# Optimization experiments

Measured on AMD Instinct MI355X. Metric: run time of the kernel, lower is better.

The kernel has to match this reference:

```python
import jax, jax.numpy as jnp
import numpy as np

EPS = 1e-5
NUM_HEADS = 8

def _bn(x, w, b, m, v):
    # inference-mode BatchNorm2d over channel dim of (B,C,H,W)
    inv = w / jnp.sqrt(v + EPS)
    return x * inv[None, :, None, None] + (b - m * inv)[None, :, None, None]

def _conv1x1(x, W, b):
    # 1x1 conv == per-pixel matmul: W is (out_ch, in_ch)
    return jnp.einsum('bchw,ec->behw', x, W) + b[None, :, None, None]

def _forward(x, bn1_w, bn1_b, bn1_m, bn1_v, Wq, bq, Wk, bk, Wv, bv, gamma, temperature,
             conv_w, conv_b, cbn_w, cbn_b, cbn_m, cbn_v, rs_w, rs_b, rbn_w, rbn_b, rbn_m, rbn_v):
    B, C, Wd, Hd = x.shape
    S = Wd * Hd
    E = Wq.shape[0]
    hd = E // NUM_HEADS
    xa = jax.nn.relu(_bn(x, bn1_w, bn1_b, bn1_m, bn1_v))
    def proj(Wm, bm):
        return _conv1x1(xa, Wm, bm).reshape(B, NUM_HEADS, hd, S).transpose(0, 1, 3, 2)  # (B,h,S,d)
    q = proj(Wq, bq)
    k = proj(Wk, bk)
    v = proj(Wv, bv)
    scores = jnp.einsum('bhsd,bhtd->bhst', q, k) / temperature  # (B,h,S,S)
    scores = scores - jnp.max(scores, axis=-1, keepdims=True)   # redundant amax-subtract as in source
    attn = jax.nn.softmax(scores, axis=-1)
    out = jnp.einsum('bhst,bhtd->bhsd', attn, v)
    out = out.transpose(0, 1, 3, 2).reshape(B, E, Wd, Hd)
    conv_path = jax.nn.relu(_bn(_conv1x1(x, conv_w, conv_b), cbn_w, cbn_b, cbn_m, cbn_v))
    fused = gamma[0] * out + conv_path
    return jax.nn.gelu(_bn(_conv1x1(fused, rs_w, rs_b), rbn_w, rbn_b, rbn_m, rbn_v), approximate=False)

def setup_inputs() -> dict:
    key = jax.random.key(0)
    ks = jax.random.split(key, 18)
    C, E = 256, 512
    n = lambda k, s, sc=0.02: jax.random.normal(k, s, jnp.float32) * sc
    return {
        'x': jax.random.normal(ks[0], (1, C, 64, 64), jnp.float32),
        'bn1_w': 1.0 + n(ks[1], (C,), 0.1), 'bn1_b': n(ks[2], (C,), 0.1),
        'bn1_m': n(ks[3], (C,), 0.05), 'bn1_v': 0.5 + jax.random.uniform(ks[4], (C,), jnp.float32),
        'Wq': n(ks[5], (E, C)), 'bq': jnp.zeros((E,), jnp.float32),
        'Wk': n(ks[6], (E, C)), 'bk': jnp.zeros((E,), jnp.float32),
        'Wv': n(ks[7], (E, C)), 'bv': jnp.zeros((E,), jnp.float32),
        'gamma': jnp.full((1,), 0.5, jnp.float32),
        'temperature': jnp.asarray(0.85, jnp.float32),
        'conv_w': n(ks[8], (E, C)), 'conv_b': jnp.zeros((E,), jnp.float32),
        'cbn_w': 1.0 + n(ks[9], (E,), 0.1), 'cbn_b': n(ks[10], (E,), 0.1),
        'cbn_m': n(ks[11], (E,), 0.05), 'cbn_v': 0.5 + jax.random.uniform(ks[12], (E,), jnp.float32),
        'rs_w': n(ks[13], (C, E)), 'rs_b': jnp.zeros((C,), jnp.float32),
        'rbn_w': 1.0 + n(ks[14], (C,), 0.1), 'rbn_b': n(ks[15], (C,), 0.1),
        'rbn_m': n(ks[16], (C,), 0.05), 'rbn_v': 0.5 + jax.random.uniform(ks[17], (C,), jnp.float32),
    }

def reference(x, bn1_w, bn1_b, bn1_m, bn1_v, Wq, bq, Wk, bk, Wv, bv, gamma, temperature,
              conv_w, conv_b, cbn_w, cbn_b, cbn_m, cbn_v, rs_w, rs_b, rbn_w, rbn_b, rbn_m, rbn_v):
    return _forward(x, bn1_w, bn1_b, bn1_m, bn1_v, Wq, bq, Wk, bk, Wv, bv, gamma, temperature,
                    conv_w, conv_b, cbn_w, cbn_b, cbn_m, cbn_v, rs_w, rs_b, rbn_w, rbn_b, rbn_m, rbn_v)
```

## Files before the change

kernel.cpp:

```cpp
#include <hip/hip_runtime.h>

#define S_DIM 4096
#define C_IN  256
#define E_DIM 512
#define HD    64
#define EPSV  1e-5f

typedef __attribute__((ext_vector_type(8))) short s8v;
typedef __attribute__((ext_vector_type(4))) short s4v;
typedef __attribute__((ext_vector_type(4))) float f4v;
typedef __attribute__((ext_vector_type(16))) float f16v;

__device__ __forceinline__ float bf2f(unsigned short h){
  union{unsigned u; float f;} v; v.u = ((unsigned)h)<<16; return v.f;
}
__device__ __forceinline__ unsigned short f2bf(float f){
  union{float f; unsigned u;} v; v.f = f;
  unsigned r = v.u + 0x7fffu + ((v.u>>16)&1u);
  return (unsigned short)(r>>16);
}
__device__ __forceinline__ unsigned cvtpk_bf16(float lo, float hi_){
  unsigned r;
  asm("v_cvt_pk_bf16_f32 %0, %1, %2" : "=v"(r) : "v"(lo), "v"(hi_));
  return r;
}
__device__ __forceinline__ s8v lds_rd8(const unsigned short* b, int row, int ck){
  return *(const s8v*)&b[(row<<6) + (((ck)^(row&7))<<3)];
}
__device__ __forceinline__ void lds_wr8(unsigned short* b, int row, int ck, s8v v){
  *(s8v*)&b[(row<<6) + (((ck)^(row&7))<<3)] = v;
}
__device__ __forceinline__ s4v lds_rd4v(const unsigned short* b, int row, int q4){
  return *(const s4v*)&b[(row<<5) + (((q4) ^ ((row>>1)&7))<<2)];
}
__device__ __forceinline__ void gl_lds16(const unsigned short* g, unsigned short* l){
  __builtin_amdgcn_global_load_lds(
      (const __attribute__((address_space(1))) unsigned int*)g,
      (__attribute__((address_space(3))) unsigned int*)l, 16, 0, 0);
}

__global__ __launch_bounds__(256) void k_wcvt(const float* __restrict__ w0,
    const float* __restrict__ w1, const float* __restrict__ w2,
    const float* __restrict__ w3, const float* __restrict__ w4,
    unsigned short* __restrict__ dst){
  int i = blockIdx.x*256 + threadIdx.x;
  int z = blockIdx.y;
  const float* s = (z==0)?w0:(z==1)?w1:(z==2)?w2:(z==3)?w3:w4;
  dst[z*(E_DIM*C_IN) + i] = f2bf(s[i]);
}

__global__ __launch_bounds__(256) void k_prep(const float* __restrict__ x,
    const float* __restrict__ bw, const float* __restrict__ bb,
    const float* __restrict__ bm, const float* __restrict__ bvar,
    unsigned short* __restrict__ XaT, unsigned short* __restrict__ XrT){
  __shared__ float tile[32][33];
  int tid = threadIdx.x;
  int tx = tid & 31, ty = tid >> 5;
  int s0 = blockIdx.x*32, c0 = blockIdx.y*32;
  #pragma unroll
  for(int p=0;p<4;p++){
    int c = c0 + ty + p*8;
    tile[ty+p*8][tx] = x[c*S_DIM + s0 + tx];
  }
  __syncthreads();
  int cc = c0 + tx;
  float inv  = bw[cc] * rsqrtf(bvar[cc] + EPSV);
  float beta = bb[cc] - bm[cc]*inv;
  #pragma unroll
  for(int p=0;p<4;p++){
    int s = s0 + ty + p*8;
    float v = tile[tx][ty+p*8];
    float a = v*inv + beta; a = a>0.f?a:0.f;
    XaT[s*C_IN + cc] = f2bf(a);
    XrT[s*C_IN + cc] = f2bf(v);
  }
}

__global__ __launch_bounds__(256) void k_proj(
    const unsigned short* __restrict__ XaT, const unsigned short* __restrict__ XrT,
    const unsigned short* __restrict__ Wb,
    const float* __restrict__ bq, const float* __restrict__ bk,
    const float* __restrict__ bvb, const float* __restrict__ bc,
    const float* __restrict__ cw, const float* __restrict__ cbb,
    const float* __restrict__ cm, const float* __restrict__ cvv,
    unsigned short* __restrict__ QT, unsigned short* __restrict__ KT,
    unsigned short* __restrict__ Vx, unsigned short* __restrict__ CT){
  int z = blockIdx.z;
  const unsigned short* Xin = (z==3) ? XrT : XaT;
  const unsigned short* W   = Wb + z*(E_DIM*C_IN);
  const float* bias = (z==0)?bq:(z==1)?bk:(z==2)?bvb:bc;

  __shared__ unsigned short Als[128*64];
  __shared__ unsigned short Bls[64*64];
  int tid = threadIdx.x;
  int w = tid>>6, l = tid&63, g = l>>4, c16 = l&15;
  int wr = w>>1, wc = w&1;
  int s0 = blockIdx.x*128, e0 = blockIdx.y*64;

  f4v acc[4][2];
  #pragma unroll
  for(int m=0;m<4;m++)
    #pragma unroll
    for(int n=0;n<2;n++) acc[m][n] = (f4v){0.f,0.f,0.f,0.f};

  for(int kk=0;kk<4;kk++){
    __syncthreads();
    #pragma unroll
    for(int p=0;p<4;p++){
      int ck = p*256 + tid, row = ck>>3, ch = ck&7;
      s8v v = *(const s8v*)&Xin[(s0+row)*C_IN + kk*64 + ch*8];
      lds_wr8(Als, row, ch, v);
    }
    #pragma unroll
    for(int p=0;p<2;p++){
      int ck = p*256 + tid, row = ck>>3, ch = ck&7;
      s8v v = *(const s8v*)&W[(e0+row)*C_IN + kk*64 + ch*8];
      lds_wr8(Bls, row, ch, v);
    }
    __syncthreads();
    #pragma unroll
    for(int kb=0;kb<2;kb++){
      s8v bfr[2];
      #pragma unroll
      for(int n=0;n<2;n++) bfr[n] = lds_rd8(Bls, wc*32 + n*16 + c16, g + kb*4);
      #pragma unroll
      for(int m=0;m<4;m++){
        s8v af = lds_rd8(Als, wr*64 + m*16 + c16, g + kb*4);
        #pragma unroll
        for(int n=0;n<2;n++)
          acc[m][n] = __builtin_amdgcn_mfma_f32_16x16x32_bf16(af, bfr[n], acc[m][n], 0,0,0);
      }
    }
  }
  #pragma unroll
  for(int n=0;n<2;n++){
    int e = e0 + wc*32 + n*16 + c16;
    float bsv = bias[e];
    float cinv = 0.f, cbeta = 0.f;
    if(z==3){ cinv = cw[e]*rsqrtf(cvv[e]+EPSV); cbeta = cbb[e] - cm[e]*cinv; }
    #pragma unroll
    for(int m=0;m<4;m++){
      int sb = s0 + wr*64 + m*16 + g*4;
      if(z==2){
        s4v pk;
        #pragma unroll
        for(int i=0;i<4;i++) pk[i] = (short)f2bf(acc[m][n][i] + bsv);
        int sb2 = (sb & ~31) | ((((sb>>2)&7) ^ ((e>>1)&7))<<2);
        *(s4v*)&Vx[e*S_DIM + sb2] = pk;
      } else {
        unsigned short* dst = (z==0)?QT:(z==1)?KT:CT;
        #pragma unroll
        for(int i=0;i<4;i++){
          float vv = acc[m][n][i] + bsv;
          if(z==3){ vv = vv*cinv + cbeta; vv = vv>0.f?vv:0.f; }
          int key = sb+i;
          int ee = e;
          if(z==1) ee = (e & ~56) | ((((e>>3)&7) ^ (key&7))<<3);
          dst[key*E_DIM + ee] = f2bf(vv);
        }
      }
    }
  }
}

__global__ __launch_bounds__(256,2) void k_attn(
    const unsigned short* __restrict__ QT, const unsigned short* __restrict__ KT,
    const unsigned short* __restrict__ Vx, const unsigned short* __restrict__ CT,
    const float* __restrict__ gamma, const float* __restrict__ temp,
    unsigned short* __restrict__ fusedT){
  __shared__ unsigned short SM[32768];
  int tid = threadIdx.x;
  int kh = tid>>6, l = tid&63, l31 = l&31, hi = l>>5;
  int bx = blockIdx.x;
  int h = bx&7;
  int q0b = (bx>>3)*64;
  float scl = 1.4426950408889634f / temp[0];

  #define STAGE(B, T) { \
    int sK = kh*1024 + (T)*32; \
    _Pragma("unroll") \
    for(int j=0;j<4;j++) \
      gl_lds16(&KT[(sK + j*8 + (l>>3))*E_DIM + h*HD + (l&7)*8], \
               SM + (B)*16384 + kh*2048 + j*512); \
    _Pragma("unroll") \
    for(int j=0;j<4;j++) \
      gl_lds16(&Vx[(h*HD + j*16 + (l>>2))*S_DIM + sK + (l&3)*8], \
               SM + (B)*16384 + 8192 + kh*2048 + j*512); \
  }

  STAGE(0, 0);

  s8v qf[2][4];
  #pragma unroll
  for(int qg=0;qg<2;qg++){
    int q = q0b + qg*32 + l31;
    #pragma unroll
    for(int ks=0;ks<4;ks++){
      s8v r = *(const s8v*)&QT[q*E_DIM + h*HD + ks*16 + hi*8];
      #pragma unroll
      for(int j=0;j<8;j++) qf[qg][ks][j] = (short)f2bf(bf2f((unsigned short)r[j])*scl);
    }
  }

  f16v oacc[2][2];
  #pragma unroll
  for(int qg=0;qg<2;qg++)
    #pragma unroll
    for(int dt=0;dt<2;dt++)
      #pragma unroll
      for(int r=0;r<16;r++) oacc[qg][dt][r]=0.f;
  float lrun[2] = {0.f, 0.f};

  int buf = 0;
  #pragma unroll 1
  for(int t=0;t<32;t++){
    if(t<31){
      STAGE(buf^1, t+1);
      asm volatile("s_waitcnt vmcnt(8)" ::: "memory");
    } else {
      asm volatile("s_waitcnt vmcnt(0)" ::: "memory");
    }
    __builtin_amdgcn_s_barrier();

    const unsigned short* Kb = SM + buf*16384 + kh*2048;
    const unsigned short* Vb = SM + buf*16384 + 8192 + kh*2048;

    s8v kf[4];
    #pragma unroll
    for(int ks=0;ks<4;ks++) kf[ks] = lds_rd8(Kb, l31, ks*2 + hi);

    union{ s8v v; unsigned u[4]; } pa[2][2];
    #pragma unroll
    for(int qg=0;qg<2;qg++){
      f16v d;
      #pragma unroll
      for(int r=0;r<16;r++) d[r]=0.f;
      __builtin_amdgcn_s_setprio(1);
      #pragma unroll
      for(int ks=0;ks<4;ks++)
        d = __builtin_amdgcn_mfma_f32_32x32x16_bf16(kf[ks], qf[qg][ks], d, 0,0,0);
      __builtin_amdgcn_s_setprio(0);
      float e_[16], ls = 0.f;
      #pragma unroll
      for(int r=0;r<16;r++){ e_[r] = __builtin_amdgcn_exp2f(d[r]); ls += e_[r]; }
      lrun[qg] += ls;
      #pragma unroll
      for(int j=0;j<4;j++){
        pa[qg][0].u[j] = cvtpk_bf16(e_[2*j],   e_[2*j+1]);
        pa[qg][1].u[j] = cvtpk_bf16(e_[8+2*j], e_[8+2*j+1]);
      }
    }

    __builtin_amdgcn_s_setprio(1);
    #pragma unroll
    for(int dt=0;dt<2;dt++){
      int vr = dt*32 + l31;
      union{ s8v v; s4v h2[2]; } vf;
      vf.h2[0] = lds_rd4v(Vb, vr, hi);
      vf.h2[1] = lds_rd4v(Vb, vr, 2 + hi);
      oacc[0][dt] = __builtin_amdgcn_mfma_f32_32x32x16_bf16(pa[0][0].v, vf.v, oacc[0][dt], 0,0,0);
      oacc[1][dt] = __builtin_amdgcn_mfma_f32_32x32x16_bf16(pa[1][0].v, vf.v, oacc[1][dt], 0,0,0);
      vf.h2[0] = lds_rd4v(Vb, vr, 4 + hi);
      vf.h2[1] = lds_rd4v(Vb, vr, 6 + hi);
      oacc[0][dt] = __builtin_amdgcn_mfma_f32_32x32x16_bf16(pa[0][1].v, vf.v, oacc[0][dt], 0,0,0);
      oacc[1][dt] = __builtin_amdgcn_mfma_f32_32x32x16_bf16(pa[1][1].v, vf.v, oacc[1][dt], 0,0,0);
    }
    __builtin_amdgcn_s_setprio(0);

    __builtin_amdgcn_sched_barrier(0);
    __builtin_amdgcn_s_barrier();
    buf ^= 1;
  }

  #pragma unroll
  for(int qg=0;qg<2;qg++) lrun[qg] += __shfl_xor(lrun[qg], 32);

  float* slab = (float*)SM;
  float* l_buf = slab + 3*64*33;
  float ga = gamma[0];
  #pragma unroll
  for(int qg=0;qg<2;qg++){
    __syncthreads();
    if(kh!=0){
      float* dst = slab + (((kh-1))*64 + l)*33;
      #pragma unroll
      for(int r=0;r<16;r++){ dst[r] = oacc[qg][0][r]; dst[16+r] = oacc[qg][1][r]; }
      dst[32] = lrun[qg];
    }
    __syncthreads();
    if(kh==0){
      float lt = lrun[qg];
      #pragma unroll
      for(int s=0;s<3;s++){
        const float* src = slab + ((s)*64 + l)*33;
        #pragma unroll
        for(int r=0;r<16;r++){ oacc[qg][0][r] += src[r]; oacc[qg][1][r] += src[16+r]; }
        lt += src[32];
      }
      if(hi==0) l_buf[l31] = lt;
      #pragma unroll
      for(int dt=0;dt<2;dt++){
        int e = h*HD + dt*32 + l31;
        #pragma unroll
        for(int g4=0;g4<4;g4++){
          float4 lv = *(float4*)&l_buf[g4*8 + hi*4];
          float la[4] = {lv.x, lv.y, lv.z, lv.w};
          #pragma unroll
          for(int j=0;j<4;j++){
            int r = g4*4 + j;
            int qrow = q0b + qg*32 + j + g4*8 + hi*4;
            float o = oacc[qg][dt][r]*(ga/la[j]) + bf2f(CT[qrow*E_DIM + e]);
            fusedT[qrow*E_DIM + e] = f2bf(o);
          }
        }
      }
    }
  }
  #undef STAGE
}

__global__ __launch_bounds__(256) void k_final(
    const unsigned short* __restrict__ Wrs,
    const unsigned short* __restrict__ fusedT,
    const float* __restrict__ rsb,
    const float* __restrict__ rw, const float* __restrict__ rbb,
    const float* __restrict__ rm, const float* __restrict__ rv,
    float* __restrict__ out){
  __shared__ unsigned short Als[64*64];
  __shared__ unsigned short Bls[64*64];
  int tid = threadIdx.x;
  int w = tid>>6, l = tid&63, g = l>>4, c16 = l&15;
  int wr2 = w>>1, wc2 = w&1;
  int sB0 = blockIdx.x*64, c0 = blockIdx.y*64;
  f4v acc[2][2];
  #pragma unroll
  for(int m=0;m<2;m++)
    #pragma unroll
    for(int n=0;n<2;n++) acc[m][n]=(f4v){0.f,0.f,0.f,0.f};
  for(int kk=0;kk<8;kk++){
    __syncthreads();
    #pragma unroll
    for(int p=0;p<2;p++){
      int ck = p*256+tid, row=ck>>3, ch=ck&7;
      s8v v = *(const s8v*)&Wrs[(c0+row)*E_DIM + kk*64 + ch*8];
      lds_wr8(Als, row, ch, v);
    }
    #pragma unroll
    for(int p=0;p<2;p++){
      int ck = p*256+tid, row=ck>>3, ch=ck&7;
      s8v v = *(const s8v*)&fusedT[(sB0+row)*E_DIM + kk*64 + ch*8];
      lds_wr8(Bls, row, ch, v);
    }
    __syncthreads();
    #pragma unroll
    for(int kb=0;kb<2;kb++){
      s8v af[2]; s8v bfr[2];
      #pragma unroll
      for(int m=0;m<2;m++) af[m] = lds_rd8(Als, wr2*32 + m*16 + c16, g + kb*4);
      #pragma unroll
      for(int n=0;n<2;n++) bfr[n] = lds_rd8(Bls, wc2*32 + n*16 + c16, g + kb*4);
      #pragma unroll
      for(int m=0;m<2;m++)
        #pragma unroll
        for(int n=0;n<2;n++)
          acc[m][n] = __builtin_amdgcn_mfma_f32_16x16x32_bf16(af[m], bfr[n], acc[m][n],0,0,0);
    }
  }
  #pragma unroll
  for(int m=0;m<2;m++){
    #pragma unroll
    for(int i=0;i<4;i++){
      int c = c0 + wr2*32 + m*16 + g*4 + i;
      float bias = rsb[c];
      float rinv = rw[c]*rsqrtf(rv[c]+EPSV);
      float rbeta = rbb[c] - rm[c]*rinv;
      #pragma unroll
      for(int n=0;n<2;n++){
        int s = sB0 + wc2*32 + n*16 + c16;
        float vv = acc[m][n][i] + bias;
        vv = vv*rinv + rbeta;
        out[c*S_DIM + s] = 0.5f*vv*(1.0f + erff(vv*0.70710678118f));
      }
    }
  }
}

extern "C" void kernel_launch(void* const* d_in, const int* in_sizes, int n_in,
                              void* d_out, int out_size, void* d_ws, size_t ws_size,
                              hipStream_t stream){
  const float* x     = (const float*)d_in[0];
  const float* bn1w  = (const float*)d_in[1];
  const float* bn1b  = (const float*)d_in[2];
  const float* bn1m  = (const float*)d_in[3];
  const float* bn1v  = (const float*)d_in[4];
  const float* Wq    = (const float*)d_in[5];
  const float* bq    = (const float*)d_in[6];
  const float* Wk    = (const float*)d_in[7];
  const float* bk    = (const float*)d_in[8];
  const float* Wv    = (const float*)d_in[9];
  const float* bv    = (const float*)d_in[10];
  const float* gamma = (const float*)d_in[11];
  const float* temp  = (const float*)d_in[12];
  const float* convw = (const float*)d_in[13];
  const float* convb = (const float*)d_in[14];
  const float* cbnw  = (const float*)d_in[15];
  const float* cbnb  = (const float*)d_in[16];
  const float* cbnm  = (const float*)d_in[17];
  const float* cbnv  = (const float*)d_in[18];
  const float* rsw   = (const float*)d_in[19];
  const float* rsbp  = (const float*)d_in[20];
  const float* rbnw  = (const float*)d_in[21];
  const float* rbnb  = (const float*)d_in[22];
  const float* rbnm  = (const float*)d_in[23];
  const float* rbnv  = (const float*)d_in[24];
  float* out = (float*)d_out;

  unsigned short* ws  = (unsigned short*)d_ws;
  unsigned short* XaT = ws;
  unsigned short* XrT = XaT + S_DIM*C_IN;
  unsigned short* Wb  = XrT + S_DIM*C_IN;
  unsigned short* Wrs = Wb + 4*E_DIM*C_IN;
  unsigned short* QT  = Wrs + C_IN*E_DIM;
  unsigned short* KT  = QT + S_DIM*E_DIM;
  unsigned short* Vx  = KT + S_DIM*E_DIM;
  unsigned short* CT  = Vx + S_DIM*E_DIM;
  unsigned short* fusedT = CT + S_DIM*E_DIM;

  k_wcvt<<<dim3(512,5),256,0,stream>>>(Wq, Wk, Wv, convw, rsw, Wb);
  k_prep<<<dim3(128,8),256,0,stream>>>(x, bn1w, bn1b, bn1m, bn1v, XaT, XrT);
  k_proj<<<dim3(32,8,4),256,0,stream>>>(XaT, XrT, Wb, bq, bk, bv, convb,
                                        cbnw, cbnb, cbnm, cbnv, QT, KT, Vx, CT);
  k_attn<<<dim3(512),256,0,stream>>>(QT, KT, Vx, CT, gamma, temp, fusedT);
  k_final<<<dim3(64,4),256,0,stream>>>(Wrs, fusedT, rsbp, rbnw, rbnb, rbnm, rbnv, out);
}
```

Baseline: 93.71 us.

## Prepack K/V into MFMA fragment layout and load directly from global, 8 waves

The projection kernel now writes K and V in a layout where each lane's MFMA operand is a contiguous 16-byte chunk. The attention kernel therefore reads fragments straight from global memory into registers, dropping the LDS double-buffered staging and its per-iteration barriers. The block grows to 512 threads (8 key-splitting waves, 16 iterations each) with a larger cross-wave reduction slab. The risk is exposed global-load latency now that there is no explicit prefetch, and scattered 2-byte stores in the projection epilogue.

```diff
diff --git a/kernel.cpp b/kernel.cpp
--- a/kernel.cpp
+++ b/kernel.cpp
@@ -29,14 +29,6 @@
 }
 __device__ __forceinline__ void lds_wr8(unsigned short* b, int row, int ck, s8v v){
   *(s8v*)&b[(row<<6) + (((ck)^(row&7))<<3)] = v;
-}
-__device__ __forceinline__ s4v lds_rd4v(const unsigned short* b, int row, int q4){
-  return *(const s4v*)&b[(row<<5) + (((q4) ^ ((row>>1)&7))<<2)];
-}
-__device__ __forceinline__ void gl_lds16(const unsigned short* g, unsigned short* l){
-  __builtin_amdgcn_global_load_lds(
-      (const __attribute__((address_space(1))) unsigned int*)g,
-      (__attribute__((address_space(3))) unsigned int*)l, 16, 0, 0);
 }
 
 __global__ __launch_bounds__(256) void k_wcvt(const float* __restrict__ w0,
@@ -83,8 +75,8 @@
     const float* __restrict__ bvb, const float* __restrict__ bc,
     const float* __restrict__ cw, const float* __restrict__ cbb,
     const float* __restrict__ cm, const float* __restrict__ cvv,
-    unsigned short* __restrict__ QT, unsigned short* __restrict__ KT,
-    unsigned short* __restrict__ Vx, unsigned short* __restrict__ CT){
+    unsigned short* __restrict__ QT, unsigned short* __restrict__ KF,
+    unsigned short* __restrict__ VF, unsigned short* __restrict__ CT){
   int z = blockIdx.z;
   const unsigned short* Xin = (z==3) ? XrT : XaT;
   const unsigned short* W   = Wb + z*(E_DIM*C_IN);
@@ -141,55 +133,43 @@
     #pragma unroll
     for(int m=0;m<4;m++){
       int sb = s0 + wr*64 + m*16 + g*4;
-      if(z==2){
-        s4v pk;
-        #pragma unroll
-        for(int i=0;i<4;i++) pk[i] = (short)f2bf(acc[m][n][i] + bsv);
-        int sb2 = (sb & ~31) | ((((sb>>2)&7) ^ ((e>>1)&7))<<2);
-        *(s4v*)&Vx[e*S_DIM + sb2] = pk;
-      } else {
-        unsigned short* dst = (z==0)?QT:(z==1)?KT:CT;
-        #pragma unroll
-        for(int i=0;i<4;i++){
-          float vv = acc[m][n][i] + bsv;
+      #pragma unroll
+      for(int i=0;i<4;i++){
+        float vv = acc[m][n][i] + bsv;
+        int key = sb+i;
+        if(z==1){
+          int hh=e>>6, d=e&63, ks=d>>4, hi8=(d>>3)&1, j=d&7;
+          int t=key>>5;
+          KF[((((hh*128+t)*4+ks)*64) + hi8*32 + (key&31))*8 + j] = f2bf(vv);
+        } else if(z==2){
+          int hh=e>>6, d=e&63, dt=d>>5, col=d&31;
+          int t=key>>5, kq=key&31, half=kq>>4, rem=kq&15;
+          int hi8=(rem>>2)&1, mm=(rem&3)+4*((rem>>3)&1);
+          VF[(((((hh*128+t)*2+dt)*2+half)*64) + hi8*32 + col)*8 + mm] = f2bf(vv);
+        } else {
           if(z==3){ vv = vv*cinv + cbeta; vv = vv>0.f?vv:0.f; }
-          int key = sb+i;
-          int ee = e;
-          if(z==1) ee = (e & ~56) | ((((e>>3)&7) ^ (key&7))<<3);
-          dst[key*E_DIM + ee] = f2bf(vv);
+          unsigned short* dst = (z==0)?QT:CT;
+          dst[key*E_DIM + e] = f2bf(vv);
         }
       }
     }
   }
 }
 
-__global__ __launch_bounds__(256,2) void k_attn(
-    const unsigned short* __restrict__ QT, const unsigned short* __restrict__ KT,
-    const unsigned short* __restrict__ Vx, const unsigned short* __restrict__ CT,
+__global__ __launch_bounds__(512,3) void k_attn(
+    const unsigned short* __restrict__ QT, const unsigned short* __restrict__ KF,
+    const unsigned short* __restrict__ VF, const unsigned short* __restrict__ CT,
     const float* __restrict__ gamma, const float* __restrict__ temp,
     unsigned short* __restrict__ fusedT){
-  __shared__ unsigned short SM[32768];
+  __shared__ float slab[7*64*33];
+  __shared__ float l_buf[32];
   int tid = threadIdx.x;
-  int kh = tid>>6, l = tid&63, l31 = l&31, hi = l>>5;
+  int w = tid>>6, l = tid&63, l31 = l&31, hi = l>>5;
   int bx = blockIdx.x;
   int h = bx&7;
   int q0b = (bx>>3)*64;
   float scl = 1.4426950408889634f / temp[0];
 
-  #define STAGE(B, T) { \
-    int sK = kh*1024 + (T)*32; \
-    _Pragma("unroll") \
-    for(int j=0;j<4;j++) \
-      gl_lds16(&KT[(sK + j*8 + (l>>3))*E_DIM + h*HD + (l&7)*8], \
-               SM + (B)*16384 + kh*2048 + j*512); \
-    _Pragma("unroll") \
-    for(int j=0;j<4;j++) \
-      gl_lds16(&Vx[(h*HD + j*16 + (l>>2))*S_DIM + sK + (l&3)*8], \
-               SM + (B)*16384 + 8192 + kh*2048 + j*512); \
-  }
-
-  STAGE(0, 0);
-
   s8v qf[2][4];
   #pragma unroll
   for(int qg=0;qg<2;qg++){
@@ -211,25 +191,17 @@
       for(int r=0;r<16;r++) oacc[qg][dt][r]=0.f;
   float lrun[2] = {0.f, 0.f};
 
-  int buf = 0;
+  const unsigned short* KFp = KF + ((h*128 + w*16)*4*64 + l)*8;
+  const unsigned short* VFp = VF + ((h*128 + w*16)*4*64 + l)*8;
+
   #pragma unroll 1
-  for(int t=0;t<32;t++){
-    if(t<31){
-      STAGE(buf^1, t+1);
-      asm volatile("s_waitcnt vmcnt(8)" ::: "memory");
-    } else {
-      asm volatile("s_waitcnt vmcnt(0)" ::: "memory");
-    }
-    __builtin_amdgcn_s_barrier();
-
-    const unsigned short* Kb = SM + buf*16384 + kh*2048;
-    const unsigned short* Vb = SM + buf*16384 + 8192 + kh*2048;
-
-    s8v kf[4];
-    #pragma unroll
-    for(int ks=0;ks<4;ks++) kf[ks] = lds_rd8(Kb, l31, ks*2 + hi);
-
-    union{ s8v v; unsigned u[4]; } pa[2][2];
+  for(int t=0;t<16;t++){
+    s8v kf[4], vf[4];
+    #pragma unroll
+    for(int i=0;i<4;i++) kf[i] = *(const s8v*)&KFp[(t*4+i)*512];
+    #pragma unroll
+    for(int i=0;i<4;i++) vf[i] = *(const s8v*)&VFp[(t*4+i)*512];
+
     #pragma unroll
     for(int qg=0;qg<2;qg++){
       f16v d;
@@ -244,55 +216,40 @@
       #pragma unroll
       for(int r=0;r<16;r++){ e_[r] = __builtin_amdgcn_exp2f(d[r]); ls += e_[r]; }
       lrun[qg] += ls;
+      union{ s8v v; unsigned u[4]; } pa0, pa1;
       #pragma unroll
       for(int j=0;j<4;j++){
-        pa[qg][0].u[j] = cvtpk_bf16(e_[2*j],   e_[2*j+1]);
-        pa[qg][1].u[j] = cvtpk_bf16(e_[8+2*j], e_[8+2*j+1]);
-      }
-    }
-
-    __builtin_amdgcn_s_setprio(1);
-    #pragma unroll
-    for(int dt=0;dt<2;dt++){
-      int vr = dt*32 + l31;
-      union{ s8v v; s4v h2[2]; } vf;
-      vf.h2[0] = lds_rd4v(Vb, vr, hi);
-      vf.h2[1] = lds_rd4v(Vb, vr, 2 + hi);
-      oacc[0][dt] = __builtin_amdgcn_mfma_f32_32x32x16_bf16(pa[0][0].v, vf.v, oacc[0][dt], 0,0,0);
-      oacc[1][dt] = __builtin_amdgcn_mfma_f32_32x32x16_bf16(pa[1][0].v, vf.v, oacc[1][dt], 0,0,0);
-      vf.h2[0] = lds_rd4v(Vb, vr, 4 + hi);
-      vf.h2[1] = lds_rd4v(Vb, vr, 6 + hi);
-      oacc[0][dt] = __builtin_amdgcn_mfma_f32_32x32x16_bf16(pa[0][1].v, vf.v, oacc[0][dt], 0,0,0);
-      oacc[1][dt] = __builtin_amdgcn_mfma_f32_32x32x16_bf16(pa[1][1].v, vf.v, oacc[1][dt], 0,0,0);
-    }
-    __builtin_amdgcn_s_setprio(0);
-
-    __builtin_amdgcn_sched_barrier(0);
-    __builtin_amdgcn_s_barrier();
-    buf ^= 1;
+        pa0.u[j] = cvtpk_bf16(e_[2*j],   e_[2*j+1]);
+        pa1.u[j] = cvtpk_bf16(e_[8+2*j], e_[8+2*j+1]);
+      }
+      __builtin_amdgcn_s_setprio(1);
+      oacc[qg][0] = __builtin_amdgcn_mfma_f32_32x32x16_bf16(pa0.v, vf[0], oacc[qg][0], 0,0,0);
+      oacc[qg][0] = __builtin_amdgcn_mfma_f32_32x32x16_bf16(pa1.v, vf[1], oacc[qg][0], 0,0,0);
+      oacc[qg][1] = __builtin_amdgcn_mfma_f32_32x32x16_bf16(pa0.v, vf[2], oacc[qg][1], 0,0,0);
+      oacc[qg][1] = __builtin_amdgcn_mfma_f32_32x32x16_bf16(pa1.v, vf[3], oacc[qg][1], 0,0,0);
+      __builtin_amdgcn_s_setprio(0);
+    }
   }
 
   #pragma unroll
   for(int qg=0;qg<2;qg++) lrun[qg] += __shfl_xor(lrun[qg], 32);
 
-  float* slab = (float*)SM;
-  float* l_buf = slab + 3*64*33;
   float ga = gamma[0];
   #pragma unroll
   for(int qg=0;qg<2;qg++){
     __syncthreads();
-    if(kh!=0){
-      float* dst = slab + (((kh-1))*64 + l)*33;
+    if(w!=0){
+      float* dst = slab + ((w-1)*64 + l)*33;
       #pragma unroll
       for(int r=0;r<16;r++){ dst[r] = oacc[qg][0][r]; dst[16+r] = oacc[qg][1][r]; }
       dst[32] = lrun[qg];
     }
     __syncthreads();
-    if(kh==0){
+    if(w==0){
       float lt = lrun[qg];
       #pragma unroll
-      for(int s=0;s<3;s++){
-        const float* src = slab + ((s)*64 + l)*33;
+      for(int s=0;s<7;s++){
+        const float* src = slab + (s*64 + l)*33;
         #pragma unroll
         for(int r=0;r<16;r++){ oacc[qg][0][r] += src[r]; oacc[qg][1][r] += src[16+r]; }
         lt += src[32];
@@ -316,7 +273,6 @@
       }
     }
   }
-  #undef STAGE
 }
 
 __global__ __launch_bounds__(256) void k_final(
@@ -421,15 +377,15 @@
   unsigned short* Wb  = XrT + S_DIM*C_IN;
   unsigned short* Wrs = Wb + 4*E_DIM*C_IN;
   unsigned short* QT  = Wrs + C_IN*E_DIM;
-  unsigned short* KT  = QT + S_DIM*E_DIM;
-  unsigned short* Vx  = KT + S_DIM*E_DIM;
-  unsigned short* CT  = Vx + S_DIM*E_DIM;
+  unsigned short* KF  = QT + S_DIM*E_DIM;
+  unsigned short* VF  = KF + S_DIM*E_DIM;
+  unsigned short* CT  = VF + S_DIM*E_DIM;
   unsigned short* fusedT = CT + S_DIM*E_DIM;
 
   k_wcvt<<<dim3(512,5),256,0,stream>>>(Wq, Wk, Wv, convw, rsw, Wb);
   k_prep<<<dim3(128,8),256,0,stream>>>(x, bn1w, bn1b, bn1m, bn1v, XaT, XrT);
   k_proj<<<dim3(32,8,4),256,0,stream>>>(XaT, XrT, Wb, bq, bk, bv, convb,
-                                        cbnw, cbnb, cbnm, cbnv, QT, KT, Vx, CT);
-  k_attn<<<dim3(512),256,0,stream>>>(QT, KT, Vx, CT, gamma, temp, fusedT);
+                                        cbnw, cbnb, cbnm, cbnv, QT, KF, VF, CT);
+  k_attn<<<dim3(512),512,0,stream>>>(QT, KF, VF, CT, gamma, temp, fusedT);
   k_final<<<dim3(64,4),256,0,stream>>>(Wrs, fusedT, rsbp, rbnw, rbnb, rbnm, rbnv, out);
 }
```

Result: slower. 149.3 us (+59.3%).
